# Optimization experiments

Measured on AMD Instinct MI355X. Metric: run time of the kernel, lower is better.

Reference implementation:

```python
import jax, jax.numpy as jnp
from jax import lax
import numpy as np

B, T, K = 256, 1024, 128


def setup_inputs() -> dict:
    key = jax.random.key(0)
    k1, k2, k3 = jax.random.split(key, 3)
    inputs = jax.random.normal(k1, (B, T, K), dtype=jnp.float32)
    transitions = jax.random.normal(k2, (K, K), dtype=jnp.float32)
    tags = jax.random.randint(k3, (B, T), 0, K, dtype=jnp.int64)
    mask = jnp.ones((B, T), dtype=jnp.int32)
    return {"inputs": inputs, "transitions": transitions, "tags": tags, "mask": mask}


def _input_likelihood(inputs, transitions, maskf):
    # inputs: [B,T,K] emissions; forward algorithm (no start/end transitions)
    emit = jnp.transpose(inputs, (1, 0, 2))  # [T,B,K]
    m = jnp.transpose(maskf, (1, 0))         # [T,B]
    alpha0 = emit[0]                          # [B,K]

    def step(alpha, xm):
        e, mi = xm  # e: [B,K], mi: [B]
        # inner[b,i,j] = alpha[b,i] + transitions[i,j] + e[b,j]
        inner = alpha[:, :, None] + transitions[None, :, :] + e[:, None, :]
        new = jax.nn.logsumexp(inner, axis=1)  # [B,K]
        alpha = new * mi[:, None] + alpha * (1.0 - mi[:, None])
        return alpha, None

    alpha, _ = lax.scan(step, alpha0, (emit[1:], m[1:]))
    return jax.nn.logsumexp(alpha, axis=-1)  # [B]


def _joint_likelihood(inputs, transitions, tags, mask, maskf):
    b, t, k = inputs.shape
    # transition scores between consecutive gold tags
    trans_scores = transitions[tags[:, :-1], tags[:, 1:]]              # [B,T-1]
    # emission scores at gold tags
    emit_scores = jnp.take_along_axis(inputs, tags[..., None], axis=2)[..., 0]  # [B,T]
    score = jnp.sum(trans_scores * maskf[:, 1:], axis=-1) \
          + jnp.sum(emit_scores[:, :-1] * maskf[:, :-1], axis=-1)
    # last valid tag's emission at the final timestep (AllenNLP semantics)
    last_idx = jnp.sum(mask, axis=1).astype(jnp.int32) - 1             # [B]
    last_tags = jnp.take_along_axis(tags, last_idx[:, None].astype(tags.dtype), axis=1)[:, 0]
    last_input_score = jnp.take_along_axis(inputs[:, -1, :], last_tags[:, None], axis=1)[:, 0]
    score = score + last_input_score * maskf[:, -1]
    return score  # [B]


def reference(inputs, transitions, tags, mask):
    maskf = mask.astype(inputs.dtype)
    log_denominator = _input_likelihood(inputs, transitions, maskf)
    log_numerator = _joint_likelihood(inputs, transitions, tags, mask, maskf)
    loglik = log_numerator - log_denominator
    return jnp.sum(loglik)  # reduction='sum'
```

## Files before the change

kernel.cpp:

```cpp
#include <hip/hip_runtime.h>
#include <math.h>

#define BB 256
#define TT 1024
#define KK 128
#define CHUNK 8
#define NCHUNK (TT / CHUNK)
#define PSTRIDE 160

__global__ void zero_out_kernel(float* out) { out[0] = 0.0f; }

#define LOBF(u) __uint_as_float((u) << 16)
#define HIBF(u) __uint_as_float((u) & 0xFFFF0000u)

#define LDE(V, I0) { V.x = expf(tcol[(size_t)(I0) * KK]); \
                     V.y = expf(tcol[(size_t)((I0) + 1) * KK]); \
                     V.z = expf(tcol[(size_t)((I0) + 2) * KK]); \
                     V.w = expf(tcol[(size_t)((I0) + 3) * KK]); }

#define FMA8(V, EA, EB) { \
    z0 = fmaf(LOBF(V.x), EA.x, z0); z1 = fmaf(HIBF(V.x), EA.y, z1); \
    z2 = fmaf(LOBF(V.y), EA.z, z2); z3 = fmaf(HIBF(V.y), EA.w, z3); \
    z0 = fmaf(LOBF(V.z), EB.x, z0); z1 = fmaf(HIBF(V.z), EB.y, z1); \
    z2 = fmaf(LOBF(V.w), EB.z, z2); z3 = fmaf(HIBF(V.w), EB.w, z3); }

__global__ __launch_bounds__(256, 1) void crf_kernel(
    const float* __restrict__ inputs,
    const float* __restrict__ trans,
    const int* __restrict__ tags,
    const int* __restrict__ mask,
    float* __restrict__ out)
{
    __shared__ __align__(16) unsigned short pbuf[2][PSTRIDE];
    __shared__ __align__(16) float ebuf[2][CHUNK * KK];
    __shared__ float mbuf[2][CHUNK];
    __shared__ float scratch[8];

    const int tid = threadIdx.x;
    const int q   = tid & 1;
    const int j   = tid >> 1;
    const int b   = blockIdx.x;

    const float* binp = inputs + (size_t)b * TT * KK;
    const int* bmask  = mask + (size_t)b * TT;
    const int* btags  = tags + (size_t)b * TT;

    const float* tcol = trans + j;
    const int ib = q * 64;
    float4 E0a, E0b, E1a, E1b, E2a, E2b, E3a, E3b, E4a, E4b, E5a, E5b, E6a, E6b, E7a, E7b;
    LDE(E0a, ib + 0)  LDE(E0b, ib + 4)
    LDE(E1a, ib + 8)  LDE(E1b, ib + 12)
    LDE(E2a, ib + 16) LDE(E2b, ib + 20)
    LDE(E3a, ib + 24) LDE(E3b, ib + 28)
    LDE(E4a, ib + 32) LDE(E4b, ib + 36)
    LDE(E5a, ib + 40) LDE(E5b, ib + 44)
    LDE(E6a, ib + 48) LDE(E6b, ib + 52)
    LDE(E7a, ib + 56) LDE(E7b, ib + 60)

    {
        float4 e4 = ((const float4*)binp)[tid];
        e4.x = __expf(e4.x); e4.y = __expf(e4.y);
        e4.z = __expf(e4.z); e4.w = __expf(e4.w);
        ((float4*)ebuf[0])[tid] = e4;
    }
    if (tid < CHUNK) mbuf[0][tid] = (float)bmask[tid];
    __syncthreads();

    float pcur = ebuf[0][j];
    int m_int = 0;
    if (q == 0) {
        unsigned bits = __float_as_uint(pcur);
        unsigned r = (bits + 0x7FFFu + ((bits >> 16) & 1u)) >> 16;
        pbuf[0][(j & 63) + ((j >> 6) * 80)] = (unsigned short)r;
    }
    __syncthreads();

    for (int c = 0; c < NCHUNK; ++c) {
        float4 epre; int mpre = 0;
        if (c + 1 < NCHUNK) {
            epre = ((const float4*)(binp + (size_t)(c + 1) * CHUNK * KK))[tid];
            if (tid < CHUNK) mpre = bmask[(c + 1) * CHUNK + tid];
        }
        const float* eb = ebuf[c & 1];
        const float* mb = mbuf[c & 1];
        const int s0 = (c == 0) ? 1 : 0;
        for (int s = s0; s < CHUNK; ++s) {
            const int t = c * CHUNK + s;
            const uint4* pr4 = (const uint4*)(pbuf[(t - 1) & 1] + q * 80);
            uint4 v0 = pr4[0], v1 = pr4[1], v2 = pr4[2], v3 = pr4[3];
            uint4 v4 = pr4[4], v5 = pr4[5], v6 = pr4[6], v7 = pr4[7];
            float z0 = 0.f, z1 = 0.f, z2 = 0.f, z3 = 0.f;
            FMA8(v0, E0a, E0b) FMA8(v1, E1a, E1b)
            FMA8(v2, E2a, E2b) FMA8(v3, E3a, E3b)
            FMA8(v4, E4a, E4b) FMA8(v5, E5a, E5b)
            FMA8(v6, E6a, E6b) FMA8(v7, E7a, E7b)
            float z = (z0 + z1) + (z2 + z3);
            z += __shfl_xor(z, 1);
            float X  = eb[s * KK + j];
            float mi = mb[s];
            float pn = (mi != 0.0f) ? z * X : pcur;
            unsigned u0 = v0.x << 16;
            int E0 = (int)((u0 >> 23) & 255u) - 127;
            float sc = __uint_as_float((unsigned)(127 - E0) << 23);
            pcur = pn * sc;
            m_int += E0;
            if (q == 0) {
                unsigned bits = __float_as_uint(pcur);
                unsigned r = (bits + 0x7FFFu + ((bits >> 16) & 1u)) >> 16;
                pbuf[t & 1][(j & 63) + ((j >> 6) * 80)] = (unsigned short)r;
            }
            __syncthreads();
        }
        if (c + 1 < NCHUNK) {
            epre.x = __expf(epre.x); epre.y = __expf(epre.y);
            epre.z = __expf(epre.z); epre.w = __expf(epre.w);
            ((float4*)ebuf[(c + 1) & 1])[tid] = epre;
            if (tid < CHUNK) mbuf[(c + 1) & 1][tid] = (float)mpre;
            __syncthreads();
        }
    }

    float a = (q == 0) ? ((float)m_int * 0.69314718055994531f + logf(pcur))
                       : -INFINITY;
    float v = a;
#pragma unroll
    for (int o = 1; o < 64; o <<= 1) v = fmaxf(v, __shfl_xor(v, o));
    if ((tid & 63) == 0) scratch[tid >> 6] = v;
    __syncthreads();
    float mx = fmaxf(fmaxf(scratch[0], scratch[1]), fmaxf(scratch[2], scratch[3]));
    float ev = (q == 0) ? __expf(a - mx) : 0.0f;
#pragma unroll
    for (int o = 1; o < 64; o <<= 1) ev += __shfl_xor(ev, o);
    __syncthreads();
    if ((tid & 63) == 0) scratch[tid >> 6] = ev;
    __syncthreads();
    float den = mx + logf((scratch[0] + scratch[1]) + (scratch[2] + scratch[3]));

    float numpart = 0.0f, maskpart = 0.0f;
#pragma unroll
    for (int kk = 0; kk < TT / 256; ++kk) {
        int t = tid + 256 * kk;
        int tg = btags[t];
        float mf = (float)bmask[t];
        maskpart += mf;
        if (t < TT - 1) {
            int tg1   = btags[t + 1];
            float mf1 = (float)bmask[t + 1];
            numpart += trans[tg * KK + tg1] * mf1;
            numpart += binp[(size_t)t * KK + tg] * mf;
        }
    }
#pragma unroll
    for (int o = 1; o < 64; o <<= 1) numpart += __shfl_xor(numpart, o);
#pragma unroll
    for (int o = 1; o < 64; o <<= 1) maskpart += __shfl_xor(maskpart, o);
    __syncthreads();
    if ((tid & 63) == 0) {
        scratch[tid >> 6]       = numpart;
        scratch[4 + (tid >> 6)] = maskpart;
    }
    __syncthreads();
    if (tid == 0) {
        float num  = (scratch[0] + scratch[1]) + (scratch[2] + scratch[3]);
        float msum = (scratch[4] + scratch[5]) + (scratch[6] + scratch[7]);
        int last_idx = (int)msum - 1;
        int ltag = btags[last_idx];
        num += binp[(size_t)(TT - 1) * KK + ltag] * (float)bmask[TT - 1];
        atomicAdd(out, num - den);
    }
}

extern "C" void kernel_launch(void* const* d_in, const int* in_sizes, int n_in,
                              void* d_out, int out_size, void* d_ws, size_t ws_size,
                              hipStream_t stream) {
    const float* inputs = (const float*)d_in[0];
    const float* trans  = (const float*)d_in[1];
    const int* tagsp    = (const int*)d_in[2];
    const int* maskp    = (const int*)d_in[3];
    float* out          = (float*)d_out;
    zero_out_kernel<<<1, 1, 0, stream>>>(out);
    crf_kernel<<<BB, 256, 0, stream>>>(inputs, trans, tagsp, maskp, out);
}
```

Before: 662.2 us.

## Split each tag's reduction across four lanes with 512-thread blocks and lighter barriers

Each output tag is now computed by four lanes instead of two, so the block grows to 512 threads and every lane does half the FMAs and LDS reads per time step, which shortens the serial per-step critical path. The chunk of prefetched emissions doubles to 16 steps, and __syncthreads is replaced by a custom barrier that waits only on LDS counters, cutting per-step sync overhead. The cost is an extra shuffle per step and a 512-thread barrier instead of a 256-thread one. Register use per thread also drops, since each lane holds half as many exp(transition) values.

```diff
diff --git a/kernel.cpp b/kernel.cpp
--- a/kernel.cpp
+++ b/kernel.cpp
@@ -4,9 +4,10 @@
 #define BB 256
 #define TT 1024
 #define KK 128
-#define CHUNK 8
+#define NTHR 512
+#define CHUNK 16
 #define NCHUNK (TT / CHUNK)
-#define PSTRIDE 160
+#define QSTR 40
 
 __global__ void zero_out_kernel(float* out) { out[0] = 0.0f; }
 
@@ -24,21 +25,25 @@
     z0 = fmaf(LOBF(V.z), EB.x, z0); z1 = fmaf(HIBF(V.z), EB.y, z1); \
     z2 = fmaf(LOBF(V.w), EB.z, z2); z3 = fmaf(HIBF(V.w), EB.w, z3); }
 
-__global__ __launch_bounds__(256, 1) void crf_kernel(
+#define BARSYNC() { asm volatile("s_waitcnt lgkmcnt(0)" ::: "memory"); \
+                    __builtin_amdgcn_s_barrier(); \
+                    asm volatile("" ::: "memory"); }
+
+__global__ __launch_bounds__(NTHR, 2) void crf_kernel(
     const float* __restrict__ inputs,
     const float* __restrict__ trans,
     const int* __restrict__ tags,
     const int* __restrict__ mask,
     float* __restrict__ out)
 {
-    __shared__ __align__(16) unsigned short pbuf[2][PSTRIDE];
+    __shared__ __align__(16) unsigned short pbuf[2][4 * QSTR];
     __shared__ __align__(16) float ebuf[2][CHUNK * KK];
     __shared__ float mbuf[2][CHUNK];
-    __shared__ float scratch[8];
+    __shared__ float scratch[16];
 
     const int tid = threadIdx.x;
-    const int q   = tid & 1;
-    const int j   = tid >> 1;
+    const int q   = tid & 3;
+    const int j   = tid >> 2;
     const int b   = blockIdx.x;
 
     const float* binp = inputs + (size_t)b * TT * KK;
@@ -46,16 +51,12 @@
     const int* btags  = tags + (size_t)b * TT;
 
     const float* tcol = trans + j;
-    const int ib = q * 64;
-    float4 E0a, E0b, E1a, E1b, E2a, E2b, E3a, E3b, E4a, E4b, E5a, E5b, E6a, E6b, E7a, E7b;
-    LDE(E0a, ib + 0)  LDE(E0b, ib + 4)
-    LDE(E1a, ib + 8)  LDE(E1b, ib + 12)
-    LDE(E2a, ib + 16) LDE(E2b, ib + 20)
-    LDE(E3a, ib + 24) LDE(E3b, ib + 28)
-    LDE(E4a, ib + 32) LDE(E4b, ib + 36)
-    LDE(E5a, ib + 40) LDE(E5b, ib + 44)
-    LDE(E6a, ib + 48) LDE(E6b, ib + 52)
-    LDE(E7a, ib + 56) LDE(E7b, ib + 60)
+    const int ib = q * 32;
+    float4 E0, E1, E2, E3, E4, E5, E6, E7;
+    LDE(E0, ib + 0)  LDE(E1, ib + 4)
+    LDE(E2, ib + 8)  LDE(E3, ib + 12)
+    LDE(E4, ib + 16) LDE(E5, ib + 20)
+    LDE(E6, ib + 24) LDE(E7, ib + 28)
 
     {
         float4 e4 = ((const float4*)binp)[tid];
@@ -64,16 +65,16 @@
         ((float4*)ebuf[0])[tid] = e4;
     }
     if (tid < CHUNK) mbuf[0][tid] = (float)bmask[tid];
-    __syncthreads();
+    BARSYNC();
 
     float pcur = ebuf[0][j];
     int m_int = 0;
     if (q == 0) {
         unsigned bits = __float_as_uint(pcur);
         unsigned r = (bits + 0x7FFFu + ((bits >> 16) & 1u)) >> 16;
-        pbuf[0][(j & 63) + ((j >> 6) * 80)] = (unsigned short)r;
+        pbuf[0][(j >> 5) * QSTR + (j & 31)] = (unsigned short)r;
     }
-    __syncthreads();
+    BARSYNC();
 
     for (int c = 0; c < NCHUNK; ++c) {
         float4 epre; int mpre = 0;
@@ -86,37 +87,35 @@
         const int s0 = (c == 0) ? 1 : 0;
         for (int s = s0; s < CHUNK; ++s) {
             const int t = c * CHUNK + s;
-            const uint4* pr4 = (const uint4*)(pbuf[(t - 1) & 1] + q * 80);
+            const uint4* pr4 = (const uint4*)(pbuf[(t - 1) & 1] + q * QSTR);
             uint4 v0 = pr4[0], v1 = pr4[1], v2 = pr4[2], v3 = pr4[3];
-            uint4 v4 = pr4[4], v5 = pr4[5], v6 = pr4[6], v7 = pr4[7];
             float z0 = 0.f, z1 = 0.f, z2 = 0.f, z3 = 0.f;
-            FMA8(v0, E0a, E0b) FMA8(v1, E1a, E1b)
-            FMA8(v2, E2a, E2b) FMA8(v3, E3a, E3b)
-            FMA8(v4, E4a, E4b) FMA8(v5, E5a, E5b)
-            FMA8(v6, E6a, E6b) FMA8(v7, E7a, E7b)
+            FMA8(v0, E0, E1) FMA8(v1, E2, E3)
+            FMA8(v2, E4, E5) FMA8(v3, E6, E7)
             float z = (z0 + z1) + (z2 + z3);
             z += __shfl_xor(z, 1);
+            z += __shfl_xor(z, 2);
             float X  = eb[s * KK + j];
             float mi = mb[s];
             float pn = (mi != 0.0f) ? z * X : pcur;
             unsigned u0 = v0.x << 16;
-            int E0 = (int)((u0 >> 23) & 255u) - 127;
-            float sc = __uint_as_float((unsigned)(127 - E0) << 23);
+            int Ex = (int)((u0 >> 23) & 255u) - 127;
+            float sc = __uint_as_float((unsigned)(127 - Ex) << 23);
             pcur = pn * sc;
-            m_int += E0;
+            m_int += Ex;
             if (q == 0) {
                 unsigned bits = __float_as_uint(pcur);
                 unsigned r = (bits + 0x7FFFu + ((bits >> 16) & 1u)) >> 16;
-                pbuf[t & 1][(j & 63) + ((j >> 6) * 80)] = (unsigned short)r;
+                pbuf[t & 1][(j >> 5) * QSTR + (j & 31)] = (unsigned short)r;
             }
-            __syncthreads();
+            BARSYNC();
         }
         if (c + 1 < NCHUNK) {
             epre.x = __expf(epre.x); epre.y = __expf(epre.y);
             epre.z = __expf(epre.z); epre.w = __expf(epre.w);
             ((float4*)ebuf[(c + 1) & 1])[tid] = epre;
             if (tid < CHUNK) mbuf[(c + 1) & 1][tid] = (float)mpre;
-            __syncthreads();
+            BARSYNC();
         }
     }
 
@@ -127,19 +126,21 @@
     for (int o = 1; o < 64; o <<= 1) v = fmaxf(v, __shfl_xor(v, o));
     if ((tid & 63) == 0) scratch[tid >> 6] = v;
     __syncthreads();
-    float mx = fmaxf(fmaxf(scratch[0], scratch[1]), fmaxf(scratch[2], scratch[3]));
+    float mx = fmaxf(fmaxf(fmaxf(scratch[0], scratch[1]), fmaxf(scratch[2], scratch[3])),
+                     fmaxf(fmaxf(scratch[4], scratch[5]), fmaxf(scratch[6], scratch[7])));
     float ev = (q == 0) ? __expf(a - mx) : 0.0f;
 #pragma unroll
     for (int o = 1; o < 64; o <<= 1) ev += __shfl_xor(ev, o);
     __syncthreads();
     if ((tid & 63) == 0) scratch[tid >> 6] = ev;
     __syncthreads();
-    float den = mx + logf((scratch[0] + scratch[1]) + (scratch[2] + scratch[3]));
+    float den = mx + logf(((scratch[0] + scratch[1]) + (scratch[2] + scratch[3]))
+                        + ((scratch[4] + scratch[5]) + (scratch[6] + scratch[7])));
 
     float numpart = 0.0f, maskpart = 0.0f;
 #pragma unroll
-    for (int kk = 0; kk < TT / 256; ++kk) {
-        int t = tid + 256 * kk;
+    for (int kk = 0; kk < TT / NTHR; ++kk) {
+        int t = tid + NTHR * kk;
         int tg = btags[t];
         float mf = (float)bmask[t];
         maskpart += mf;
@@ -157,12 +158,14 @@
     __syncthreads();
     if ((tid & 63) == 0) {
         scratch[tid >> 6]       = numpart;
-        scratch[4 + (tid >> 6)] = maskpart;
+        scratch[8 + (tid >> 6)] = maskpart;
     }
     __syncthreads();
     if (tid == 0) {
-        float num  = (scratch[0] + scratch[1]) + (scratch[2] + scratch[3]);
-        float msum = (scratch[4] + scratch[5]) + (scratch[6] + scratch[7]);
+        float num  = ((scratch[0] + scratch[1]) + (scratch[2] + scratch[3]))
+                   + ((scratch[4] + scratch[5]) + (scratch[6] + scratch[7]));
+        float msum = ((scratch[8] + scratch[9]) + (scratch[10] + scratch[11]))
+                   + ((scratch[12] + scratch[13]) + (scratch[14] + scratch[15]));
         int last_idx = (int)msum - 1;
         int ltag = btags[last_idx];
         num += binp[(size_t)(TT - 1) * KK + ltag] * (float)bmask[TT - 1];
@@ -179,5 +182,5 @@
     const int* maskp    = (const int*)d_in[3];
     float* out          = (float*)d_out;
     zero_out_kernel<<<1, 1, 0, stream>>>(out);
-    crf_kernel<<<BB, 256, 0, stream>>>(inputs, trans, tagsp, maskp, out);
+    crf_kernel<<<BB, NTHR, 0, stream>>>(inputs, trans, tagsp, maskp, out);
 }
```

Result: faster. 645.6 us (-2.5%).
